# Performance work log

Hardware: AMD Instinct MI355X
Metric: run time of the kernel (lower is better)

Reference implementation:

```python
import jax, jax.numpy as jnp
import numpy as np

N, E, G = 50000, 1600000, 8
IN, H, C = 64, 4, 32
HID = H * C  # 128
L = 3


def setup_inputs() -> dict:
    key = jax.random.key(0)
    ks = jax.random.split(key, 20)
    x = jax.random.normal(ks[0], (N, IN), dtype=jnp.float32)
    edge_index = jax.random.randint(ks[1], (2, E), 0, N, dtype=jnp.int64)
    batch = jnp.sort(jax.random.randint(ks[2], (N,), 0, G, dtype=jnp.int64))
    s = 0.05
    Wp = jax.random.normal(ks[3], (IN, HID), dtype=jnp.float32) * s
    bp = jnp.zeros((HID,), dtype=jnp.float32)
    Wl = jax.random.normal(ks[4], (L, HID, HID), dtype=jnp.float32) * s
    att_src = jax.random.normal(ks[5], (L, H, C), dtype=jnp.float32) * s
    att_dst = jax.random.normal(ks[6], (L, H, C), dtype=jnp.float32) * s
    bconv = jnp.zeros((L, HID), dtype=jnp.float32)
    W1 = jax.random.normal(ks[7], (2 * HID, 256), dtype=jnp.float32) * s
    b1 = jnp.zeros((256,), dtype=jnp.float32)
    W2 = jax.random.normal(ks[8], (256, 128), dtype=jnp.float32) * s
    b2 = jnp.zeros((128,), dtype=jnp.float32)
    W3 = jax.random.normal(ks[9], (128, 1), dtype=jnp.float32) * s
    b3 = jnp.zeros((1,), dtype=jnp.float32)
    return dict(x=x, edge_index=edge_index, batch=batch, Wp=Wp, bp=bp, Wl=Wl,
                att_src=att_src, att_dst=att_dst, bconv=bconv,
                W1=W1, b1=b1, W2=W2, b2=b2, W3=W3, b3=b3)


def _gat_layer(x, src, dst, W, a_src, a_dst, b):
    # PyG GATConv (concat=True, add_self_loops handled by caller via src/dst)
    h = (x @ W).reshape(N, H, C)                      # [N,H,C]
    asrc = jnp.sum(h * a_src, axis=-1)                # [N,H]
    adst = jnp.sum(h * a_dst, axis=-1)                # [N,H]
    e = jax.nn.leaky_relu(asrc[src] + adst[dst], 0.2)  # [E',H]
    m = jax.ops.segment_max(e, dst, num_segments=N)   # scatter-softmax over dst
    e = jnp.exp(e - m[dst])
    z = jax.ops.segment_sum(e, dst, num_segments=N)
    alpha = e / (z[dst] + 1e-16)                      # [E',H]
    out = jax.ops.segment_sum(h[src] * alpha[:, :, None], dst, num_segments=N)
    return out.reshape(N, HID) + b


def reference(x, edge_index, batch, Wp, bp, Wl, att_src, att_dst, bconv,
              W1, b1, W2, b2, W3, b3):
    # add self loops once (PyG default add_self_loops=True)
    loop = jnp.arange(N, dtype=edge_index.dtype)
    src = jnp.concatenate([edge_index[0], loop])
    dst = jnp.concatenate([edge_index[1], loop])

    h = jax.nn.relu(x @ Wp + bp)
    for l in range(L):
        h = jax.nn.relu(_gat_layer(h, src, dst, Wl[l], att_src[l], att_dst[l], bconv[l]))

    cnt = jax.ops.segment_sum(jnp.ones((N,), h.dtype), batch, num_segments=G)
    mean = jax.ops.segment_sum(h, batch, num_segments=G) / jnp.maximum(cnt, 1.0)[:, None]
    mx = jax.ops.segment_max(h, batch, num_segments=G)
    mx = jnp.where(cnt[:, None] > 0, mx, 0.0)
    p = jnp.concatenate([mean, mx], axis=-1)          # [G, 2*HID]

    p = jax.nn.relu(p @ W1 + b1)
    p = jax.nn.relu(p @ W2 + b2)
    return (p @ W3 + b3).squeeze(-1)                  # [G]
```

## Files before the change

### kernel.cpp

```cpp
#include <hip/hip_runtime.h>
#include <math.h>

#define NN 50000
#define GG 8
#define HEADS 4
#define CH 32
#define HID 128
#define NLAYER 3
#define POOL_S 64
#define DEG_CAP 96
#define NBG2 ((NN + 63) / 64)
#define NBS 1024

typedef __attribute__((ext_vector_type(8))) short bf16x8;
typedef __attribute__((ext_vector_type(4))) float f32x4;

__device__ float g_h[(size_t)NN * HID];
__device__ __attribute__((aligned(16))) unsigned short g_h2b[(size_t)NN * HID];
__device__ __attribute__((aligned(16))) unsigned short g_xhi[(size_t)NN * HID];
__device__ __attribute__((aligned(16))) unsigned short g_xlo[(size_t)NN * HID];
__device__ __attribute__((aligned(16))) unsigned short g_wthi[(size_t)NLAYER * HID * HID];
__device__ __attribute__((aligned(16))) unsigned short g_wtlo[(size_t)NLAYER * HID * HID];
__device__ float g_as[(size_t)NN * HEADS];
__device__ float g_ad[(size_t)NN * HEADS];
__device__ int g_cursor[NN];
__device__ __attribute__((aligned(16))) unsigned short g_csr16[(size_t)NN * DEG_CAP];
__device__ int g_starts[GG + 1];
__device__ double g_psum[(size_t)GG * POOL_S * HID];
__device__ float g_pmax[(size_t)GG * POOL_S * HID];

__device__ __forceinline__ float lrelu(float v) { return v > 0.f ? v : 0.2f * v; }

__device__ __forceinline__ float bf2f(unsigned short u) {
    union { unsigned int i; float f; } v;
    v.i = ((unsigned int)u) << 16;
    return v.f;
}
__device__ __forceinline__ unsigned short f2bf(float f) {
    union { float f; unsigned int i; } v;
    v.f = f;
    unsigned int r = v.i + 0x7FFFu + ((v.i >> 16) & 1u);
    return (unsigned short)(r >> 16);
}

__global__ void zero_kernel() {
    int i = blockIdx.x * blockDim.x + threadIdx.x;
    if (i < NN) g_cursor[i] = 0;
}

__global__ void wprep_kernel(const float* __restrict__ Wl) {
    int idx = blockIdx.x * 256 + threadIdx.x;
    if (idx >= NLAYER * HID * HID) return;
    int lay = idx / (HID * HID);
    int rem = idx - lay * HID * HID;
    int n = rem >> 7, k = rem & 127;
    float v = Wl[(size_t)lay * HID * HID + (size_t)k * HID + n];
    unsigned short h = f2bf(v);
    float r = v - bf2f(h);
    g_wthi[idx] = h;
    g_wtlo[idx] = f2bf(r);
}

template <int K>
__device__ __forceinline__ void proj_body(
    const float* __restrict__ Xp, const float* __restrict__ W, const float* __restrict__ bias,
    int blk) {
    constexpr int KT = 32;
    constexpr int XS = 68;
    __shared__ float Ws[KT * 128];
    __shared__ float Xs[KT * XS];
    int tid = threadIdx.x;
    int base = blk * 64;
    int rows = NN - base;
    if (rows > 64) rows = 64;
    int cg = tid & 15, rg = tid >> 4;
    int c0 = cg * 8, r0 = rg * 4;
    float acc[4][8];
#pragma unroll
    for (int i = 0; i < 4; i++)
#pragma unroll
        for (int j = 0; j < 8; j++) acc[i][j] = 0.f;

    for (int kb = 0; kb < K; kb += KT) {
        {
            const float4* Wg = (const float4*)(W + (size_t)kb * 128);
            float4* Ws4 = (float4*)Ws;
#pragma unroll
            for (int u = 0; u < 4; u++) Ws4[tid + u * 256] = Wg[tid + u * 256];
        }
#pragma unroll
        for (int u = 0; u < 2; u++) {
            int i = tid + u * 256;
            int r = i >> 3, k4 = i & 7;
            float4 v = {0.f, 0.f, 0.f, 0.f};
            if (r < rows) v = *(const float4*)(Xp + (size_t)(base + r) * K + kb + k4 * 4);
            Xs[(k4 * 4 + 0) * XS + r] = v.x;
            Xs[(k4 * 4 + 1) * XS + r] = v.y;
            Xs[(k4 * 4 + 2) * XS + r] = v.z;
            Xs[(k4 * 4 + 3) * XS + r] = v.w;
        }
        __syncthreads();
#pragma unroll 8
        for (int k = 0; k < KT; k++) {
            const float4 xa = *(const float4*)&Xs[k * XS + r0];
            const float4 wa = *(const float4*)&Ws[k * 128 + c0];
            const float4 wb = *(const float4*)&Ws[k * 128 + c0 + 4];
            const float xr[4] = {xa.x, xa.y, xa.z, xa.w};
            const float wr[8] = {wa.x, wa.y, wa.z, wa.w, wb.x, wb.y, wb.z, wb.w};
#pragma unroll
            for (int ii = 0; ii < 4; ii++)
#pragma unroll
                for (int jj = 0; jj < 8; jj++) acc[ii][jj] += xr[ii] * wr[jj];
        }
        __syncthreads();
    }

    float bv[8];
#pragma unroll
    for (int j = 0; j < 8; j++) bv[j] = bias[c0 + j];
#pragma unroll
    for (int ii = 0; ii < 4; ii++) {
        int r = r0 + ii;
        if (r < rows) {
            ushort4 h0, l0, h1, l1;
            float o[8];
#pragma unroll
            for (int jj = 0; jj < 8; jj++) o[jj] = fmaxf(acc[ii][jj] + bv[jj], 0.f);
            h0.x = f2bf(o[0]); h0.y = f2bf(o[1]); h0.z = f2bf(o[2]); h0.w = f2bf(o[3]);
            h1.x = f2bf(o[4]); h1.y = f2bf(o[5]); h1.z = f2bf(o[6]); h1.w = f2bf(o[7]);
            l0.x = f2bf(o[0] - bf2f(h0.x)); l0.y = f2bf(o[1] - bf2f(h0.y));
            l0.z = f2bf(o[2] - bf2f(h0.z)); l0.w = f2bf(o[3] - bf2f(h0.w));
            l1.x = f2bf(o[4] - bf2f(h1.x)); l1.y = f2bf(o[5] - bf2f(h1.y));
            l1.z = f2bf(o[6] - bf2f(h1.z)); l1.w = f2bf(o[7] - bf2f(h1.w));
            size_t off = (size_t)(base + r) * 128 + c0;
            *(ushort4*)&g_xhi[off] = h0;
            *(ushort4*)&g_xhi[off + 4] = h1;
            *(ushort4*)&g_xlo[off] = l0;
            *(ushort4*)&g_xlo[off + 4] = l1;
        }
    }
}

__device__ __forceinline__ void scatter_body(
    const int* __restrict__ srcv, const int* __restrict__ dstv, int ebeg, int eend,
    int blk, int nblk) {
    int stride = nblk * 256;
    int j = ebeg + blk * 256 + threadIdx.x;
    for (; j + 7 * stride < eend; j += 8 * stride) {
        int d[8], s[8], p[8];
#pragma unroll
        for (int u = 0; u < 8; ++u) {
            d[u] = dstv[j + u * stride];
            s[u] = srcv[j + u * stride];
        }
#pragma unroll
        for (int u = 0; u < 8; ++u) p[u] = atomicAdd(&g_cursor[d[u]], 1);
#pragma unroll
        for (int u = 0; u < 8; ++u)
            if (p[u] < DEG_CAP) g_csr16[(size_t)d[u] * DEG_CAP + p[u]] = (unsigned short)s[u];
    }
    for (; j < eend; j += stride) {
        int d = dstv[j];
        int pos = atomicAdd(&g_cursor[d], 1);
        if (pos < DEG_CAP) g_csr16[(size_t)d * DEG_CAP + pos] = (unsigned short)srcv[j];
    }
}

__device__ __forceinline__ void mfma_att_body(
    const float* __restrict__ att_s, const float* __restrict__ att_d, int lay, int blk) {
    __shared__ float Ysh[64][HID];
    int tid = threadIdx.x;
    int w = tid >> 6, l = tid & 63;
    int base = blk * 64;
    int rows = NN - base;
    if (rows > 64) rows = 64;
    int ar = l & 15, kg = l >> 4;
    int arow = base + w * 16 + ar;
    if (arow >= NN) arow = NN - 1;
    const unsigned short* xh = g_xhi + (size_t)arow * HID + kg * 8;
    const unsigned short* xl = g_xlo + (size_t)arow * HID + kg * 8;
    const unsigned short* wh = g_wthi + (size_t)lay * HID * HID + (size_t)ar * HID + kg * 8;
    const unsigned short* wl = g_wtlo + (size_t)lay * HID * HID + (size_t)ar * HID + kg * 8;

    f32x4 acc[8];
#pragma unroll
    for (int ct = 0; ct < 8; ct++) acc[ct] = (f32x4){0.f, 0.f, 0.f, 0.f};

#pragma unroll
    for (int ks = 0; ks < 4; ks++) {
        bf16x8 ah = *(const bf16x8*)(xh + ks * 32);
        bf16x8 al = *(const bf16x8*)(xl + ks * 32);
#pragma unroll
        for (int ct = 0; ct < 8; ct++) {
            bf16x8 bh = *(const bf16x8*)(wh + ct * 16 * HID + ks * 32);
            bf16x8 bl = *(const bf16x8*)(wl + ct * 16 * HID + ks * 32);
            acc[ct] = __builtin_amdgcn_mfma_f32_16x16x32_bf16(ah, bh, acc[ct], 0, 0, 0);
            acc[ct] = __builtin_amdgcn_mfma_f32_16x16x32_bf16(al, bh, acc[ct], 0, 0, 0);
            acc[ct] = __builtin_amdgcn_mfma_f32_16x16x32_bf16(ah, bl, acc[ct], 0, 0, 0);
        }
    }

#pragma unroll
    for (int ct = 0; ct < 8; ct++)
#pragma unroll
        for (int j = 0; j < 4; j++)
            Ysh[w * 16 + kg * 4 + j][ct * 16 + ar] = acc[ct][j];
    __syncthreads();

    int cg = tid & 15, rg = tid >> 4;
    int c0 = cg * 8, r0 = rg * 4;
    float avs[8], avd[8];
#pragma unroll
    for (int j = 0; j < 8; j++) { avs[j] = att_s[c0 + j]; avd[j] = att_d[c0 + j]; }
#pragma unroll
    for (int ii = 0; ii < 4; ii++) {
        int r = r0 + ii;
        float o[8];
#pragma unroll
        for (int jj = 0; jj < 8; jj++) o[jj] = Ysh[r][c0 + jj];
        if (r < rows) {
            uint4 pk;
            pk.x = (unsigned)f2bf(o[0]) | ((unsigned)f2bf(o[1]) << 16);
            pk.y = (unsigned)f2bf(o[2]) | ((unsigned)f2bf(o[3]) << 16);
            pk.z = (unsigned)f2bf(o[4]) | ((unsigned)f2bf(o[5]) << 16);
            pk.w = (unsigned)f2bf(o[6]) | ((unsigned)f2bf(o[7]) << 16);
            *(uint4*)&g_h2b[(size_t)(base + r) * 128 + c0] = pk;
        }
        float ps = 0.f, pd = 0.f;
#pragma unroll
        for (int jj = 0; jj < 8; jj++) { ps += o[jj] * avs[jj]; pd += o[jj] * avd[jj]; }
        ps += __shfl_xor(ps, 1); ps += __shfl_xor(ps, 2);
        pd += __shfl_xor(pd, 1); pd += __shfl_xor(pd, 2);
        if ((cg & 3) == 0 && r < rows) {
            g_as[(size_t)(base + r) * 4 + (cg >> 2)] = ps;
            g_ad[(size_t)(base + r) * 4 + (cg >> 2)] = pd;
        }
    }
}

__global__ __launch_bounds__(256) void fat1_kernel(
    const float* __restrict__ Xp, const float* __restrict__ W, const float* __restrict__ bias,
    const int* __restrict__ srcv, const int* __restrict__ dstv, int ebeg, int eend) {
    if (blockIdx.x < NBG2) proj_body<64>(Xp, W, bias, blockIdx.x);
    else scatter_body(srcv, dstv, ebeg, eend, blockIdx.x - NBG2, NBS);
}

__global__ __launch_bounds__(256, 2) void fat2_kernel(
    const float* __restrict__ att_s, const float* __restrict__ att_d,
    const int* __restrict__ srcv, const int* __restrict__ dstv, int ebeg, int eend) {
    if (blockIdx.x < NBG2) mfma_att_body(att_s, att_d, 0, blockIdx.x);
    else scatter_body(srcv, dstv, ebeg, eend, blockIdx.x - NBG2, NBS);
}

__global__ __launch_bounds__(256, 2) void att_gemm_kernel(
    const float* __restrict__ att_s, const float* __restrict__ att_d, int lay) {
    mfma_att_body(att_s, att_d, lay, blockIdx.x);
}

template <bool LAST>
__global__ __launch_bounds__(256) void gat_layer_kernel(const float* __restrict__ bconv) {
    int wave = threadIdx.x >> 6;
    int lane = threadIdx.x & 63;
    int i = blockIdx.x * 4 + wave;

    int deg = g_cursor[i];
    if (deg > DEG_CAP) deg = DEG_CAP;

    int stream = lane >> 5;
    int sl = lane & 31;
    int hl = sl >> 3;
    int li = sl & 7;
    int c0 = sl * 4;
    int bsel = lane & 56;

    float ad_h = g_ad[(size_t)i * 4 + hl];
    const unsigned short* csr = &g_csr16[(size_t)i * DEG_CAP];

    float4 acc = {0.f, 0.f, 0.f, 0.f};
    float zraw = 0.f;

    int nfull = deg >> 4;
    for (int t = 0; t < nfull; ++t) {
        int j0 = t * 16 + stream * 8;
        uint4 cs = *(const uint4*)(csr + j0);
        int s0 = cs.x & 0xFFFF, s1 = cs.x >> 16;
        int s2 = cs.y & 0xFFFF, s3 = cs.y >> 16;
        int s4 = cs.z & 0xFFFF, s5 = cs.z >> 16;
        int s6 = cs.w & 0xFFFF, s7 = cs.w >> 16;
        ushort4 q0 = *(const ushort4*)&g_h2b[(s0 << 7) + c0];
        ushort4 q1 = *(const ushort4*)&g_h2b[(s1 << 7) + c0];
        ushort4 q2 = *(const ushort4*)&g_h2b[(s2 << 7) + c0];
        ushort4 q3 = *(const ushort4*)&g_h2b[(s3 << 7) + c0];
        ushort4 q4 = *(const ushort4*)&g_h2b[(s4 << 7) + c0];
        ushort4 q5 = *(const ushort4*)&g_h2b[(s5 << 7) + c0];
        ushort4 q6 = *(const ushort4*)&g_h2b[(s6 << 7) + c0];
        ushort4 q7 = *(const ushort4*)&g_h2b[(s7 << 7) + c0];
        unsigned wsel = li < 4 ? (li < 2 ? cs.x : cs.y) : (li < 6 ? cs.z : cs.w);
        int sm = (li & 1) ? (int)(wsel >> 16) : (int)(wsel & 0xFFFF);
        float a = g_as[(sm << 2) + hl];
        float wr = expf(lrelu(a + ad_h));
        zraw += wr;
        float w0 = __shfl(wr, bsel | 0);
        float w1 = __shfl(wr, bsel | 1);
        float w2 = __shfl(wr, bsel | 2);
        float w3 = __shfl(wr, bsel | 3);
        float w4 = __shfl(wr, bsel | 4);
        float w5 = __shfl(wr, bsel | 5);
        float w6 = __shfl(wr, bsel | 6);
        float w7 = __shfl(wr, bsel | 7);
        acc.x += w0 * bf2f(q0.x); acc.y += w0 * bf2f(q0.y); acc.z += w0 * bf2f(q0.z); acc.w += w0 * bf2f(q0.w);
        acc.x += w1 * bf2f(q1.x); acc.y += w1 * bf2f(q1.y); acc.z += w1 * bf2f(q1.z); acc.w += w1 * bf2f(q1.w);
        acc.x += w2 * bf2f(q2.x); acc.y += w2 * bf2f(q2.y); acc.z += w2 * bf2f(q2.z); acc.w += w2 * bf2f(q2.w);
        acc.x += w3 * bf2f(q3.x); acc.y += w3 * bf2f(q3.y); acc.z += w3 * bf2f(q3.z); acc.w += w3 * bf2f(q3.w);
        acc.x += w4 * bf2f(q4.x); acc.y += w4 * bf2f(q4.y); acc.z += w4 * bf2f(q4.z); acc.w += w4 * bf2f(q4.w);
        acc.x += w5 * bf2f(q5.x); acc.y += w5 * bf2f(q5.y); acc.z += w5 * bf2f(q5.z); acc.w += w5 * bf2f(q5.w);
        acc.x += w6 * bf2f(q6.x); acc.y += w6 * bf2f(q6.y); acc.z += w6 * bf2f(q6.z); acc.w += w6 * bf2f(q6.w);
        acc.x += w7 * bf2f(q7.x); acc.y += w7 * bf2f(q7.y); acc.z += w7 * bf2f(q7.z); acc.w += w7 * bf2f(q7.w);
    }

    int tbase = nfull * 16 + stream * 8;
#pragma unroll
    for (int k = 0; k < 8; ++k) {
        if (tbase + k < deg) {
            int s = csr[tbase + k];
            float a = g_as[(s << 2) + hl];
            float wr = expf(lrelu(a + ad_h));
            zraw += wr * 0.125f;
            ushort4 q = *(const ushort4*)&g_h2b[(s << 7) + c0];
            acc.x += wr * bf2f(q.x); acc.y += wr * bf2f(q.y);
            acc.z += wr * bf2f(q.z); acc.w += wr * bf2f(q.w);
        }
    }

    acc.x += __shfl_xor(acc.x, 32);
    acc.y += __shfl_xor(acc.y, 32);
    acc.z += __shfl_xor(acc.z, 32);
    acc.w += __shfl_xor(acc.w, 32);
    zraw += __shfl_xor(zraw, 1);
    zraw += __shfl_xor(zraw, 2);
    zraw += __shfl_xor(zraw, 4);
    zraw += __shfl_xor(zraw, 32);

    if (lane < 32) {
        float as_i = g_as[(i << 2) + hl];
        float sw = expf(lrelu(as_i + ad_h));
        float invz = 1.f / (zraw + sw + 1e-16f);
        ushort4 qs = *(const ushort4*)&g_h2b[(i << 7) + c0];
        float4 bc = *(const float4*)&bconv[c0];
        float4 o;
        o.x = fmaxf((sw * bf2f(qs.x) + acc.x) * invz + bc.x, 0.f);
        o.y = fmaxf((sw * bf2f(qs.y) + acc.y) * invz + bc.y, 0.f);
        o.z = fmaxf((sw * bf2f(qs.z) + acc.z) * invz + bc.z, 0.f);
        o.w = fmaxf((sw * bf2f(qs.w) + acc.w) * invz + bc.w, 0.f);
        if (LAST) {
            *(float4*)&g_h[(size_t)i * 128 + c0] = o;
        } else {
            ushort4 hh, ll;
            hh.x = f2bf(o.x); hh.y = f2bf(o.y); hh.z = f2bf(o.z); hh.w = f2bf(o.w);
            ll.x = f2bf(o.x - bf2f(hh.x)); ll.y = f2bf(o.y - bf2f(hh.y));
            ll.z = f2bf(o.z - bf2f(hh.z)); ll.w = f2bf(o.w - bf2f(hh.w));
            *(ushort4*)&g_xhi[(size_t)i * 128 + c0] = hh;
            *(ushort4*)&g_xlo[(size_t)i * 128 + c0] = ll;
        }
    }
}

__global__ void bounds_kernel(const int* __restrict__ batch) {
    int t = threadIdx.x;
    if (t > GG) return;
    int lo = 0, hi = NN;
    while (lo < hi) {
        int mid = (lo + hi) >> 1;
        if (batch[mid] < t) lo = mid + 1; else hi = mid;
    }
    g_starts[t] = lo;
}

__global__ void pool1_kernel() {
    int g = blockIdx.x / POOL_S, s = blockIdx.x % POOL_S;
    int n0 = g_starts[g], n1 = g_starts[g + 1];
    long long cnt = n1 - n0;
    int a = n0 + (int)(cnt * s / POOL_S);
    int b = n0 + (int)(cnt * (s + 1) / POOL_S);
    int c = threadIdx.x;
    double sum = 0.0;
    float mx = -INFINITY;
    for (int nn = a; nn < b; nn++) {
        float v = g_h[(size_t)nn * 128 + c];
        sum += v;
        mx = fmaxf(mx, v);
    }
    g_psum[(size_t)blockIdx.x * 128 + c] = sum;
    g_pmax[(size_t)blockIdx.x * 128 + c] = mx;
}

__global__ __launch_bounds__(256) void head_kernel(
    const float* __restrict__ W1, const float* __restrict__ b1,
    const float* __restrict__ W2, const float* __restrict__ b2,
    const float* __restrict__ W3, const float* __restrict__ b3,
    float* __restrict__ outv) {
    __shared__ float p[256];
    __shared__ float r1[256];
    __shared__ float r2[128];
    int g = blockIdx.x, t = threadIdx.x;
    int cnt = g_starts[g + 1] - g_starts[g];
    if (t < 128) {
        double s = 0.0;
        for (int q = 0; q < POOL_S; q++) s += g_psum[(size_t)(g * POOL_S + q) * 128 + t];
        double dcnt = cnt > 0 ? (double)cnt : 1.0;
        p[t] = (float)(s / dcnt);
    } else {
        int c = t - 128;
        float mx = -INFINITY;
        for (int q = 0; q < POOL_S; q++) mx = fmaxf(mx, g_pmax[(size_t)(g * POOL_S + q) * 128 + c]);
        p[t] = cnt > 0 ? mx : 0.f;
    }
    __syncthreads();
    float acc = b1[t];
    for (int k = 0; k < 256; k++) acc += p[k] * W1[k * 256 + t];
    r1[t] = fmaxf(acc, 0.f);
    __syncthreads();
    if (t < 128) {
        float a2 = b2[t];
        for (int k = 0; k < 256; k++) a2 += r1[k] * W2[k * 128 + t];
        r2[t] = fmaxf(a2, 0.f);
    }
    __syncthreads();
    if (t < 64) {
        float a3 = r2[t] * W3[t] + r2[t + 64] * W3[t + 64];
#pragma unroll
        for (int d = 32; d >= 1; d >>= 1) a3 += __shfl_down(a3, d);
        if (t == 0) outv[g] = a3 + b3[0];
    }
}

extern "C" void kernel_launch(void* const* d_in, const int* in_sizes, int n_in,
                              void* d_out, int out_size, void* d_ws, size_t ws_size,
                              hipStream_t stream) {
    const float* x = (const float*)d_in[0];
    const int* eidx = (const int*)d_in[1];
    const int* batch = (const int*)d_in[2];
    const float* Wp = (const float*)d_in[3];
    const float* bp = (const float*)d_in[4];
    const float* Wl = (const float*)d_in[5];
    const float* att_src = (const float*)d_in[6];
    const float* att_dst = (const float*)d_in[7];
    const float* bconv = (const float*)d_in[8];
    const float* W1 = (const float*)d_in[9];
    const float* b1 = (const float*)d_in[10];
    const float* W2 = (const float*)d_in[11];
    const float* b2 = (const float*)d_in[12];
    const float* W3 = (const float*)d_in[13];
    const float* b3 = (const float*)d_in[14];
    float* out = (float*)d_out;
    int E = in_sizes[1] / 2;
    int Emid = E / 2;

    zero_kernel<<<(NN + 255) / 256, 256, 0, stream>>>();
    wprep_kernel<<<(NLAYER * HID * HID + 255) / 256, 256, 0, stream>>>(Wl);

    fat1_kernel<<<NBG2 + NBS, 256, 0, stream>>>(x, Wp, bp, eidx, eidx + E, 0, Emid);

    fat2_kernel<<<NBG2 + NBS, 256, 0, stream>>>(att_src, att_dst, eidx, eidx + E, Emid, E);

    gat_layer_kernel<false><<<NN / 4, 256, 0, stream>>>(bconv);

    att_gemm_kernel<<<NBG2, 256, 0, stream>>>(
        att_src + (size_t)1 * HID, att_dst + (size_t)1 * HID, 1);
    gat_layer_kernel<false><<<NN / 4, 256, 0, stream>>>(bconv + (size_t)1 * HID);

    att_gemm_kernel<<<NBG2, 256, 0, stream>>>(
        att_src + (size_t)2 * HID, att_dst + (size_t)2 * HID, 2);
    gat_layer_kernel<true><<<NN / 4, 256, 0, stream>>>(bconv + (size_t)2 * HID);

    bounds_kernel<<<1, 64, 0, stream>>>(batch);
    pool1_kernel<<<GG * POOL_S, 128, 0, stream>>>();
    head_kernel<<<GG, 256, 0, stream>>>(W1, b1, W2, b2, W3, b3, out);
}
```

Before: 548.9 us.

## Fuse GAT layers, pooling and head into one cooperative persistent kernel

```diff
diff --git a/kernel.cpp b/kernel.cpp
--- a/kernel.cpp
+++ b/kernel.cpp
@@ -1,4 +1,5 @@
 #include <hip/hip_runtime.h>
+#include <hip/hip_cooperative_groups.h>
 #include <math.h>
 
 #define NN 50000
@@ -25,7 +26,6 @@
 __device__ float g_ad[(size_t)NN * HEADS];
 __device__ int g_cursor[NN];
 __device__ __attribute__((aligned(16))) unsigned short g_csr16[(size_t)NN * DEG_CAP];
-__device__ int g_starts[GG + 1];
 __device__ double g_psum[(size_t)GG * POOL_S * HID];
 __device__ float g_pmax[(size_t)GG * POOL_S * HID];
 
@@ -43,22 +43,19 @@
     return (unsigned short)(r >> 16);
 }
 
-__global__ void zero_kernel() {
+__global__ void init_kernel(const float* __restrict__ Wl) {
     int i = blockIdx.x * blockDim.x + threadIdx.x;
     if (i < NN) g_cursor[i] = 0;
-}
-
-__global__ void wprep_kernel(const float* __restrict__ Wl) {
-    int idx = blockIdx.x * 256 + threadIdx.x;
-    if (idx >= NLAYER * HID * HID) return;
-    int lay = idx / (HID * HID);
-    int rem = idx - lay * HID * HID;
-    int n = rem >> 7, k = rem & 127;
-    float v = Wl[(size_t)lay * HID * HID + (size_t)k * HID + n];
-    unsigned short h = f2bf(v);
-    float r = v - bf2f(h);
-    g_wthi[idx] = h;
-    g_wtlo[idx] = f2bf(r);
+    if (i < NLAYER * HID * HID) {
+        int lay = i / (HID * HID);
+        int rem = i - lay * HID * HID;
+        int n = rem >> 7, k = rem & 127;
+        float v = Wl[(size_t)lay * HID * HID + (size_t)k * HID + n];
+        unsigned short h = f2bf(v);
+        float r = v - bf2f(h);
+        g_wthi[i] = h;
+        g_wtlo[i] = f2bf(r);
+    }
 }
 
 template <int K>
@@ -200,6 +197,7 @@
         }
     }
 
+    __syncthreads();
 #pragma unroll
     for (int ct = 0; ct < 8; ct++)
 #pragma unroll
@@ -252,16 +250,11 @@
     else scatter_body(srcv, dstv, ebeg, eend, blockIdx.x - NBG2, NBS);
 }
 
-__global__ __launch_bounds__(256, 2) void att_gemm_kernel(
-    const float* __restrict__ att_s, const float* __restrict__ att_d, int lay) {
-    mfma_att_body(att_s, att_d, lay, blockIdx.x);
-}
-
 template <bool LAST>
-__global__ __launch_bounds__(256) void gat_layer_kernel(const float* __restrict__ bconv) {
+__device__ __forceinline__ void gat_body(const float* __restrict__ bconv, int grp) {
     int wave = threadIdx.x >> 6;
     int lane = threadIdx.x & 63;
-    int i = blockIdx.x * 4 + wave;
+    int i = grp * 4 + wave;
 
     int deg = g_cursor[i];
     if (deg > DEG_CAP) deg = DEG_CAP;
@@ -365,45 +358,17 @@
     }
 }
 
-__global__ void bounds_kernel(const int* __restrict__ batch) {
-    int t = threadIdx.x;
-    if (t > GG) return;
-    int lo = 0, hi = NN;
-    while (lo < hi) {
-        int mid = (lo + hi) >> 1;
-        if (batch[mid] < t) lo = mid + 1; else hi = mid;
-    }
-    g_starts[t] = lo;
-}
-
-__global__ void pool1_kernel() {
-    int g = blockIdx.x / POOL_S, s = blockIdx.x % POOL_S;
-    int n0 = g_starts[g], n1 = g_starts[g + 1];
-    long long cnt = n1 - n0;
-    int a = n0 + (int)(cnt * s / POOL_S);
-    int b = n0 + (int)(cnt * (s + 1) / POOL_S);
-    int c = threadIdx.x;
-    double sum = 0.0;
-    float mx = -INFINITY;
-    for (int nn = a; nn < b; nn++) {
-        float v = g_h[(size_t)nn * 128 + c];
-        sum += v;
-        mx = fmaxf(mx, v);
-    }
-    g_psum[(size_t)blockIdx.x * 128 + c] = sum;
-    g_pmax[(size_t)blockIdx.x * 128 + c] = mx;
-}
-
-__global__ __launch_bounds__(256) void head_kernel(
+__device__ __forceinline__ void head_body(
+    const int* __restrict__ sstarts,
     const float* __restrict__ W1, const float* __restrict__ b1,
     const float* __restrict__ W2, const float* __restrict__ b2,
     const float* __restrict__ W3, const float* __restrict__ b3,
-    float* __restrict__ outv) {
+    float* __restrict__ outv, int g) {
     __shared__ float p[256];
     __shared__ float r1[256];
     __shared__ float r2[128];
-    int g = blockIdx.x, t = threadIdx.x;
-    int cnt = g_starts[g + 1] - g_starts[g];
+    int t = threadIdx.x;
+    int cnt = sstarts[g + 1] - sstarts[g];
     if (t < 128) {
         double s = 0.0;
         for (int q = 0; q < POOL_S; q++) s += g_psum[(size_t)(g * POOL_S + q) * 128 + t];
@@ -432,6 +397,64 @@
         for (int d = 32; d >= 1; d >>= 1) a3 += __shfl_down(a3, d);
         if (t == 0) outv[g] = a3 + b3[0];
     }
+}
+
+__global__ __launch_bounds__(256) void coop_kernel(
+    const float* __restrict__ att_src, const float* __restrict__ att_dst,
+    const float* __restrict__ bconv, const int* __restrict__ batch,
+    const float* __restrict__ W1, const float* __restrict__ b1,
+    const float* __restrict__ W2, const float* __restrict__ b2,
+    const float* __restrict__ W3, const float* __restrict__ b3,
+    float* __restrict__ outv) {
+    cooperative_groups::grid_group grid = cooperative_groups::this_grid();
+    int nb = gridDim.x;
+
+    for (int g = blockIdx.x; g < NN / 4; g += nb) gat_body<false>(bconv, g);
+    grid.sync();
+    for (int t = blockIdx.x; t < NBG2; t += nb)
+        mfma_att_body(att_src + HID, att_dst + HID, 1, t);
+    grid.sync();
+    for (int g = blockIdx.x; g < NN / 4; g += nb) gat_body<false>(bconv + HID, g);
+    grid.sync();
+    for (int t = blockIdx.x; t < NBG2; t += nb)
+        mfma_att_body(att_src + 2 * HID, att_dst + 2 * HID, 2, t);
+    grid.sync();
+    for (int g = blockIdx.x; g < NN / 4; g += nb) gat_body<true>(bconv + 2 * HID, g);
+    grid.sync();
+
+    __shared__ int sstarts[GG + 1];
+    if (threadIdx.x <= GG) {
+        int tt = threadIdx.x, lo = 0, hi = NN;
+        while (lo < hi) {
+            int mid = (lo + hi) >> 1;
+            if (batch[mid] < tt) lo = mid + 1; else hi = mid;
+        }
+        sstarts[tt] = lo;
+    }
+    __syncthreads();
+    int half = threadIdx.x >> 7;
+    int c = threadIdx.x & 127;
+    for (int it = blockIdx.x; it < (GG * POOL_S) / 2; it += nb) {
+        int slice = it * 2 + half;
+        int g = slice / POOL_S, s = slice % POOL_S;
+        int n0 = sstarts[g], n1 = sstarts[g + 1];
+        long long cnt = n1 - n0;
+        int a = n0 + (int)(cnt * s / POOL_S);
+        int b = n0 + (int)(cnt * (s + 1) / POOL_S);
+        double sum = 0.0;
+        float mx = -INFINITY;
+        for (int nn = a; nn < b; nn++) {
+            float v = g_h[(size_t)nn * 128 + c];
+            sum += v;
+            mx = fmaxf(mx, v);
+        }
+        g_psum[(size_t)slice * 128 + c] = sum;
+        g_pmax[(size_t)slice * 128 + c] = mx;
+    }
+    grid.sync();
+
+    if (blockIdx.x < GG)
+        head_body(sstarts, W1, b1, W2, b2, W3, b3, outv, blockIdx.x);
 }
 
 extern "C" void kernel_launch(void* const* d_in, const int* in_sizes, int n_in,
@@ -456,24 +479,25 @@
     int E = in_sizes[1] / 2;
     int Emid = E / 2;
 
-    zero_kernel<<<(NN + 255) / 256, 256, 0, stream>>>();
-    wprep_kernel<<<(NLAYER * HID * HID + 255) / 256, 256, 0, stream>>>(Wl);
+    init_kernel<<<(NN + 255) / 256, 256, 0, stream>>>(Wl);
 
     fat1_kernel<<<NBG2 + NBS, 256, 0, stream>>>(x, Wp, bp, eidx, eidx + E, 0, Emid);
 
     fat2_kernel<<<NBG2 + NBS, 256, 0, stream>>>(att_src, att_dst, eidx, eidx + E, Emid, E);
 
-    gat_layer_kernel<false><<<NN / 4, 256, 0, stream>>>(bconv);
-
-    att_gemm_kernel<<<NBG2, 256, 0, stream>>>(
-        att_src + (size_t)1 * HID, att_dst + (size_t)1 * HID, 1);
-    gat_layer_kernel<false><<<NN / 4, 256, 0, stream>>>(bconv + (size_t)1 * HID);
-
-    att_gemm_kernel<<<NBG2, 256, 0, stream>>>(
-        att_src + (size_t)2 * HID, att_dst + (size_t)2 * HID, 2);
-    gat_layer_kernel<true><<<NN / 4, 256, 0, stream>>>(bconv + (size_t)2 * HID);
-
-    bounds_kernel<<<1, 64, 0, stream>>>(batch);
-    pool1_kernel<<<GG * POOL_S, 128, 0, stream>>>();
-    head_kernel<<<GG, 256, 0, stream>>>(W1, b1, W2, b2, W3, b3, out);
-}
+    static int coop_grid = 0;
+    if (coop_grid == 0) {
+        int maxb = 0;
+        if (hipOccupancyMaxActiveBlocksPerMultiprocessor(&maxb, coop_kernel, 256, 0) != hipSuccess
+            || maxb < 1)
+            maxb = 2;
+        coop_grid = maxb * 256;
+        if (coop_grid > 2048) coop_grid = 2048;
+        if (coop_grid < 256) coop_grid = 256;
+    }
+    void* cargs[] = {(void*)&att_src, (void*)&att_dst, (void*)&bconv, (void*)&batch,
+                     (void*)&W1, (void*)&b1, (void*)&W2, (void*)&b2,
+                     (void*)&W3, (void*)&b3, (void*)&out};
+    hipLaunchCooperativeKernel(reinterpret_cast<void*>(coop_kernel),
+                               dim3(coop_grid), dim3(256), cargs, 0, stream);
+}
```

New measurement: 1.338 ms. 144% more time.
